# Kernel tuning notes

Measured on AMD Instinct MI355X. Metric: run time of the kernel, lower is better.

The kernel has to match this reference:

```python
import jax, jax.numpy as jnp
import numpy as np

VOCABSIZE = 100000
EMBEDSIZE = 128
BATCH = 262144


def setup_inputs() -> dict:
    key = jax.random.key(0)
    k1, k2, k3, k4, k5 = jax.random.split(key, 5)
    xs = jax.random.randint(k1, (BATCH,), 0, VOCABSIZE, dtype=jnp.int64 if jax.config.jax_enable_x64 else jnp.int32)
    ys = jax.random.randint(k2, (BATCH,), 0, VOCABSIZE, dtype=jnp.int64 if jax.config.jax_enable_x64 else jnp.int32)
    metric = jax.random.normal(k3, (EMBEDSIZE, EMBEDSIZE), dtype=jnp.float32)
    EMBEDM = jax.random.normal(k4, (VOCABSIZE, EMBEDSIZE), dtype=jnp.float32)
    # Original inits NEGEMBEDM to zeros; we use small random values so the
    # output / gradients are non-degenerate for kernel correctness testing.
    NEGEMBEDM = jax.random.normal(k5, (VOCABSIZE, EMBEDSIZE), dtype=jnp.float32) * 0.1
    return {"xs": xs, "ys": ys, "metric": metric, "EMBEDM": EMBEDM, "NEGEMBEDM": NEGEMBEDM}


def reference(xs, ys, metric, EMBEDM, NEGEMBEDM):
    # Faithful math: diag((E[xs] @ metric) @ N[ys].T) == sum((E[xs] @ metric) * N[ys], -1).
    # We compute the batched bilinear form directly, avoiding the O(B^2*D)
    # full matmul + diag extraction of the original.
    xsembeds = EMBEDM[xs]          # [B, D]
    ysembeds = NEGEMBEDM[ys]       # [B, D]
    d = jnp.einsum('bd,de,be->b', xsembeds, metric, ysembeds)  # [B]
    return jax.nn.sigmoid(2.0 * d - 1.0)
```

## Files before the change

### kernel.cpp

```cpp
#include <hip/hip_runtime.h>
#include <hip/hip_fp16.h>

#define D       128
#define NROWS   100000
#define NTILES  (NROWS / 16)
#define NBE     391
#define NBN     (NROWS / 16)
#define NPREP   (NBE + NBN)

typedef __attribute__((ext_vector_type(8))) _Float16 f16x8;
typedef __attribute__((ext_vector_type(4))) float    f32x4;

union F16x8U { _Float16 h[8]; f16x8 v; };
union F32x4U { float f[4]; f32x4 v; };

typedef __attribute__((address_space(1))) const void gvoid;
typedef __attribute__((address_space(3))) void       lvoid;

__global__ __launch_bounds__(256) void convert_M16(
    const float* __restrict__ M, _Float16* __restrict__ mh)
{
    const int q    = blockIdx.x * 256 + threadIdx.x;
    const int kk   = q >> 9;
    const int cf   = (q >> 6) & 7;
    const int lane = q & 63;
    const int col  = cf * 16 + (lane & 15);
    const int k0   = kk * 32 + (lane >> 4) * 8;

    F16x8U h;
    #pragma unroll
    for (int j = 0; j < 8; ++j) h.h[j] = (_Float16)M[(k0 + j) * D + col];
    *(f16x8*)(mh + q * 8) = h.v;
}

__global__ __launch_bounds__(256, 5) void prep_fused(
    const float* __restrict__ E, const float* __restrict__ N,
    const _Float16* __restrict__ mh,
    _Float16* __restrict__ Ep, _Float16* __restrict__ Np)
{
    __shared__ _Float16 sm[2048 * 8];

    const int tid = threadIdx.x;
    const int bid = (int)blockIdx.x;

    if (bid % 17 != 0) {
        const int nid = bid - bid / 17 - 1;
        const int l16 = tid & 15;
        const int row = nid * 16 + (tid >> 4);
        const float* src = N + (size_t)row * D + l16;
        F16x8U o;
        #pragma unroll
        for (int k = 0; k < 8; ++k) o.h[k] = (_Float16)src[16 * k];
        *(f16x8*)(Np + (size_t)row * D + l16 * 8) = o.v;
        return;
    }

    const int eid  = bid / 17;
    const int lane = tid & 63;
    const int w    = tid >> 6;
    const int lrow = lane & 15;
    const int lk   = lane >> 4;

    #pragma unroll
    for (int it = 0; it < 8; ++it) {
        const int slot = it * 256 + w * 64 + lane;
        __builtin_amdgcn_global_load_lds(
            (gvoid*)(mh + slot * 8), (lvoid*)(sm + (it * 256 + w * 64) * 8),
            16, 0, 0);
    }
    asm volatile("s_waitcnt vmcnt(0)" ::: "memory");
    __syncthreads();

    const f16x8* Bh = (const f16x8*)sm;

    #pragma unroll 1
    for (int rt = 0; rt < 4; ++rt) {
        const int tb = eid * 16 + rt * 4 + w;
        if (tb >= NTILES) break;
        const int row = tb * 16 + lrow;

        f32x4 ax[4], ay[4];
        #pragma unroll
        for (int kk = 0; kk < 4; ++kk) {
            const float* p = E + (size_t)row * D + kk * 32 + lk * 8;
            ax[kk] = *(const f32x4*)p;
            ay[kk] = *(const f32x4*)(p + 4);
        }

        f32x4 acc[8];
        #pragma unroll
        for (int cf = 0; cf < 8; ++cf) acc[cf] = (f32x4){0.f, 0.f, 0.f, 0.f};

        #pragma unroll
        for (int kk = 0; kk < 4; ++kk) {
            F16x8U a16;
            F32x4U x, y; x.v = ax[kk]; y.v = ay[kk];
            #pragma unroll
            for (int j = 0; j < 4; ++j) {
                a16.h[j]     = (_Float16)x.f[j];
                a16.h[j + 4] = (_Float16)y.f[j];
            }
            #pragma unroll
            for (int cf = 0; cf < 8; ++cf)
                acc[cf] = __builtin_amdgcn_mfma_f32_16x16x32_f16(
                    a16.v, Bh[(kk * 8 + cf) * 64 + lane], acc[cf], 0, 0, 0);
        }

        #pragma unroll
        for (int i = 0; i < 4; ++i) {
            const int ro = tb * 16 + lk * 4 + i;
            F16x8U o;
            #pragma unroll
            for (int cf = 0; cf < 8; ++cf) o.h[cf] = (_Float16)acc[cf][i];
            *(f16x8*)(Ep + (size_t)ro * D + lrow * 8) = o.v;
        }
    }
}

__global__ __launch_bounds__(256) void gather_dot16(
    const int* __restrict__ xs, const int* __restrict__ ys,
    const _Float16* __restrict__ Ep, const _Float16* __restrict__ Np,
    float* __restrict__ out)
{
    const int tid = threadIdx.x;
    const int o0  = blockIdx.x * 32 + (tid >> 4) * 2;
    const int l   = tid & 15;

    const int x0 = xs[o0], x1 = xs[o0 + 1];
    const int y0 = ys[o0], y1 = ys[o0 + 1];

    const f16x8 a0 = *(const f16x8*)(Ep + (size_t)x0 * D + l * 8);
    const f16x8 b0 = *(const f16x8*)(Np + (size_t)y0 * D + l * 8);
    const f16x8 a1 = *(const f16x8*)(Ep + (size_t)x1 * D + l * 8);
    const f16x8 b1 = *(const f16x8*)(Np + (size_t)y1 * D + l * 8);

    float r0 = 0.f, r1 = 0.f;
    #pragma unroll
    for (int j = 0; j < 8; ++j) {
        r0 += (float)a0[j] * (float)b0[j];
        r1 += (float)a1[j] * (float)b1[j];
    }

    r0 += __shfl_xor(r0, 1); r1 += __shfl_xor(r1, 1);
    r0 += __shfl_xor(r0, 2); r1 += __shfl_xor(r1, 2);
    r0 += __shfl_xor(r0, 4); r1 += __shfl_xor(r1, 4);
    r0 += __shfl_xor(r0, 8); r1 += __shfl_xor(r1, 8);

    if (l == 0) {
        float2 v;
        v.x = 1.0f / (1.0f + __expf(1.0f - 2.0f * r0));
        v.y = 1.0f / (1.0f + __expf(1.0f - 2.0f * r1));
        *(float2*)(out + o0) = v;
    }
}

extern "C" void kernel_launch(void* const* d_in, const int* in_sizes, int n_in,
                              void* d_out, int out_size, void* d_ws, size_t ws_size,
                              hipStream_t stream) {
    const int*   xs     = (const int*)d_in[0];
    const int*   ys     = (const int*)d_in[1];
    const float* metric = (const float*)d_in[2];
    const float* EMBEDM = (const float*)d_in[3];
    const float* NEGEM  = (const float*)d_in[4];
    float*       out    = (float*)d_out;

    const int B = in_sizes[0];

    char* ws = (char*)d_ws;
    _Float16* Np = (_Float16*)ws;
    _Float16* Ep = (_Float16*)(ws + (32u << 20));
    _Float16* mh = (_Float16*)(ws + (64u << 20));

    convert_M16<<<8, 256, 0, stream>>>(metric, mh);

    prep_fused<<<NPREP, 256, 0, stream>>>(EMBEDM, NEGEM, mh, Ep, Np);

    gather_dot16<<<B / 32, 256, 0, stream>>>(xs, ys, Ep, Np, out);
}
```

Measured before the change: 56.27 us.

## Use persistent grid-stride waves for fused E-projection and N-conversion prep

Replaces the one-block-per-work-item prep launch with a fixed 1280-block persistent grid. Each wave strides over a unified list of work units: E tiles that need the MFMA projection, then N row-quads that only need fp16 conversion. The goal is to cut block launch overhead and spread the heavier MFMA tiles across all waves. In exchange, every block now loads the 32KB metric into LDS even if it mostly does N conversion, and the E tiles all come first in the list, which may unbalance work or hurt overlap.

```diff
diff --git a/kernel.cpp b/kernel.cpp
--- a/kernel.cpp
+++ b/kernel.cpp
@@ -1,12 +1,13 @@
 #include <hip/hip_runtime.h>
 #include <hip/hip_fp16.h>
 
-#define D       128
-#define NROWS   100000
-#define NTILES  (NROWS / 16)
-#define NBE     391
-#define NBN     (NROWS / 16)
-#define NPREP   (NBE + NBN)
+#define D        128
+#define NROWS    100000
+#define NET      (NROWS / 16)
+#define NNT      (NROWS / 4)
+#define NUNITS   (NET + NNT)
+#define GRID_P   1280
+#define NWAVES   (GRID_P * 4)
 
 typedef __attribute__((ext_vector_type(8))) _Float16 f16x8;
 typedef __attribute__((ext_vector_type(4))) float    f32x4;
@@ -33,29 +34,14 @@
     *(f16x8*)(mh + q * 8) = h.v;
 }
 
-__global__ __launch_bounds__(256, 5) void prep_fused(
+__global__ __launch_bounds__(256, 5) void prep_all(
     const float* __restrict__ E, const float* __restrict__ N,
     const _Float16* __restrict__ mh,
     _Float16* __restrict__ Ep, _Float16* __restrict__ Np)
 {
     __shared__ _Float16 sm[2048 * 8];
 
-    const int tid = threadIdx.x;
-    const int bid = (int)blockIdx.x;
-
-    if (bid % 17 != 0) {
-        const int nid = bid - bid / 17 - 1;
-        const int l16 = tid & 15;
-        const int row = nid * 16 + (tid >> 4);
-        const float* src = N + (size_t)row * D + l16;
-        F16x8U o;
-        #pragma unroll
-        for (int k = 0; k < 8; ++k) o.h[k] = (_Float16)src[16 * k];
-        *(f16x8*)(Np + (size_t)row * D + l16 * 8) = o.v;
-        return;
-    }
-
-    const int eid  = bid / 17;
+    const int tid  = threadIdx.x;
     const int lane = tid & 63;
     const int w    = tid >> 6;
     const int lrow = lane & 15;
@@ -73,46 +59,55 @@
 
     const f16x8* Bh = (const f16x8*)sm;
 
+    const int gwave = (int)blockIdx.x * 4 + w;
+
     #pragma unroll 1
-    for (int rt = 0; rt < 4; ++rt) {
-        const int tb = eid * 16 + rt * 4 + w;
-        if (tb >= NTILES) break;
-        const int row = tb * 16 + lrow;
+    for (int u = gwave; u < NUNITS; u += NWAVES) {
+        if (u < NET) {
+            const int row = u * 16 + lrow;
 
-        f32x4 ax[4], ay[4];
-        #pragma unroll
-        for (int kk = 0; kk < 4; ++kk) {
-            const float* p = E + (size_t)row * D + kk * 32 + lk * 8;
-            ax[kk] = *(const f32x4*)p;
-            ay[kk] = *(const f32x4*)(p + 4);
-        }
+            f32x4 ax[4], ay[4];
+            #pragma unroll
+            for (int kk = 0; kk < 4; ++kk) {
+                const float* p = E + (size_t)row * D + kk * 32 + lk * 8;
+                ax[kk] = *(const f32x4*)p;
+                ay[kk] = *(const f32x4*)(p + 4);
+            }
 
-        f32x4 acc[8];
-        #pragma unroll
-        for (int cf = 0; cf < 8; ++cf) acc[cf] = (f32x4){0.f, 0.f, 0.f, 0.f};
+            f32x4 acc[8];
+            #pragma unroll
+            for (int cf = 0; cf < 8; ++cf) acc[cf] = (f32x4){0.f, 0.f, 0.f, 0.f};
 
-        #pragma unroll
-        for (int kk = 0; kk < 4; ++kk) {
-            F16x8U a16;
-            F32x4U x, y; x.v = ax[kk]; y.v = ay[kk];
             #pragma unroll
-            for (int j = 0; j < 4; ++j) {
-                a16.h[j]     = (_Float16)x.f[j];
-                a16.h[j + 4] = (_Float16)y.f[j];
+            for (int kk = 0; kk < 4; ++kk) {
+                F16x8U a16;
+                F32x4U x, y; x.v = ax[kk]; y.v = ay[kk];
+                #pragma unroll
+                for (int j = 0; j < 4; ++j) {
+                    a16.h[j]     = (_Float16)x.f[j];
+                    a16.h[j + 4] = (_Float16)y.f[j];
+                }
+                #pragma unroll
+                for (int cf = 0; cf < 8; ++cf)
+                    acc[cf] = __builtin_amdgcn_mfma_f32_16x16x32_f16(
+                        a16.v, Bh[(kk * 8 + cf) * 64 + lane], acc[cf], 0, 0, 0);
             }
+
             #pragma unroll
-            for (int cf = 0; cf < 8; ++cf)
-                acc[cf] = __builtin_amdgcn_mfma_f32_16x16x32_f16(
-                    a16.v, Bh[(kk * 8 + cf) * 64 + lane], acc[cf], 0, 0, 0);
-        }
-
-        #pragma unroll
-        for (int i = 0; i < 4; ++i) {
-            const int ro = tb * 16 + lk * 4 + i;
+            for (int i = 0; i < 4; ++i) {
+                const int ro = u * 16 + lk * 4 + i;
+                F16x8U o;
+                #pragma unroll
+                for (int cf = 0; cf < 8; ++cf) o.h[cf] = (_Float16)acc[cf][i];
+                *(f16x8*)(Ep + (size_t)ro * D + lrow * 8) = o.v;
+            }
+        } else {
+            const int row = (u - NET) * 4 + lk;
+            const float* src = N + (size_t)row * D + lrow;
             F16x8U o;
             #pragma unroll
-            for (int cf = 0; cf < 8; ++cf) o.h[cf] = (_Float16)acc[cf][i];
-            *(f16x8*)(Ep + (size_t)ro * D + lrow * 8) = o.v;
+            for (int k = 0; k < 8; ++k) o.h[k] = (_Float16)src[16 * k];
+            *(f16x8*)(Np + (size_t)row * D + lrow * 8) = o.v;
         }
     }
 }
@@ -173,7 +168,7 @@
 
     convert_M16<<<8, 256, 0, stream>>>(metric, mh);
 
-    prep_fused<<<NPREP, 256, 0, stream>>>(EMBEDM, NEGEM, mh, Ep, Np);
+    prep_all<<<GRID_P, 256, 0, stream>>>(EMBEDM, NEGEM, mh, Ep, Np);
 
     gather_dot16<<<B / 32, 256, 0, stream>>>(xs, ys, Ep, Np, out);
 }
```

New measurement: 53.07 us. 1.06x faster.

## Split fused prep into separate E-GEMM and N-convert kernels with finer GEMM work split

Applied to the files above, without the earlier changes.

Replaces the interleaved fused prep kernel with two launches: a GEMM kernel for E·M using 512-thread blocks where each tile's 8 output column fragments are split across two waves, and a standalone fp16 conversion kernel for N. Each E block now handles 4 tiles in a single pass instead of looping over 16 tiles, so there are more blocks and more waves and less serial work per block. The cost is an extra kernel launch, and the metric matrix is now loaded into LDS by more blocks in total.

```diff
diff --git a/kernel.cpp b/kernel.cpp
--- a/kernel.cpp
+++ b/kernel.cpp
@@ -3,15 +3,16 @@
 
 #define D       128
 #define NROWS   100000
-#define NTILES  (NROWS / 16)
-#define NBE     391
+#define NET     (NROWS / 16)
+#define NBE     ((NET + 3) / 4)
 #define NBN     (NROWS / 16)
-#define NPREP   (NBE + NBN)
 
 typedef __attribute__((ext_vector_type(8))) _Float16 f16x8;
+typedef __attribute__((ext_vector_type(4))) _Float16 f16x4;
 typedef __attribute__((ext_vector_type(4))) float    f32x4;
 
 union F16x8U { _Float16 h[8]; f16x8 v; };
+union F16x4U { _Float16 h[4]; f16x4 v; };
 union F32x4U { float f[4]; f32x4 v; };
 
 typedef __attribute__((address_space(1))) const void gvoid;
@@ -33,88 +34,79 @@
     *(f16x8*)(mh + q * 8) = h.v;
 }
 
-__global__ __launch_bounds__(256, 5) void prep_fused(
-    const float* __restrict__ E, const float* __restrict__ N,
-    const _Float16* __restrict__ mh,
-    _Float16* __restrict__ Ep, _Float16* __restrict__ Np)
+__global__ __launch_bounds__(512, 8) void gemm_E_hi(
+    const float* __restrict__ E, const _Float16* __restrict__ mh,
+    _Float16* __restrict__ Ep)
 {
-    __shared__ _Float16 sm[2048 * 8];
+    __shared__ _Float16 smM[2048 * 8];
 
-    const int tid = threadIdx.x;
-    const int bid = (int)blockIdx.x;
-
-    if (bid % 17 != 0) {
-        const int nid = bid - bid / 17 - 1;
-        const int l16 = tid & 15;
-        const int row = nid * 16 + (tid >> 4);
-        const float* src = N + (size_t)row * D + l16;
-        F16x8U o;
-        #pragma unroll
-        for (int k = 0; k < 8; ++k) o.h[k] = (_Float16)src[16 * k];
-        *(f16x8*)(Np + (size_t)row * D + l16 * 8) = o.v;
-        return;
-    }
-
-    const int eid  = bid / 17;
+    const int tid  = threadIdx.x;
     const int lane = tid & 63;
     const int w    = tid >> 6;
     const int lrow = lane & 15;
     const int lk   = lane >> 4;
 
     #pragma unroll
-    for (int it = 0; it < 8; ++it) {
-        const int slot = it * 256 + w * 64 + lane;
+    for (int it = 0; it < 4; ++it) {
+        const int slot = it * 512 + w * 64 + lane;
         __builtin_amdgcn_global_load_lds(
-            (gvoid*)(mh + slot * 8), (lvoid*)(sm + (it * 256 + w * 64) * 8),
+            (gvoid*)(mh + slot * 8), (lvoid*)(smM + (it * 512 + w * 64) * 8),
             16, 0, 0);
     }
     asm volatile("s_waitcnt vmcnt(0)" ::: "memory");
     __syncthreads();
 
-    const f16x8* Bh = (const f16x8*)sm;
+    const f16x8* Bh = (const f16x8*)smM;
 
-    #pragma unroll 1
-    for (int rt = 0; rt < 4; ++rt) {
-        const int tb = eid * 16 + rt * 4 + w;
-        if (tb >= NTILES) break;
-        const int row = tb * 16 + lrow;
+    const int tile = (int)blockIdx.x * 4 + (w >> 1);
+    if (tile >= NET) return;
+    const int h   = w & 1;
+    const int row = tile * 16 + lrow;
 
-        f32x4 ax[4], ay[4];
+    f32x4 acc[4];
+    #pragma unroll
+    for (int c = 0; c < 4; ++c) acc[c] = (f32x4){0.f, 0.f, 0.f, 0.f};
+
+    #pragma unroll
+    for (int kk = 0; kk < 4; ++kk) {
+        const float* p = E + (size_t)row * D + kk * 32 + lk * 8;
+        F32x4U x, y;
+        x.v = *(const f32x4*)p;
+        y.v = *(const f32x4*)(p + 4);
+        F16x8U a16;
         #pragma unroll
-        for (int kk = 0; kk < 4; ++kk) {
-            const float* p = E + (size_t)row * D + kk * 32 + lk * 8;
-            ax[kk] = *(const f32x4*)p;
-            ay[kk] = *(const f32x4*)(p + 4);
+        for (int j = 0; j < 4; ++j) {
+            a16.h[j]     = (_Float16)x.f[j];
+            a16.h[j + 4] = (_Float16)y.f[j];
         }
-
-        f32x4 acc[8];
         #pragma unroll
-        for (int cf = 0; cf < 8; ++cf) acc[cf] = (f32x4){0.f, 0.f, 0.f, 0.f};
-
-        #pragma unroll
-        for (int kk = 0; kk < 4; ++kk) {
-            F16x8U a16;
-            F32x4U x, y; x.v = ax[kk]; y.v = ay[kk];
-            #pragma unroll
-            for (int j = 0; j < 4; ++j) {
-                a16.h[j]     = (_Float16)x.f[j];
-                a16.h[j + 4] = (_Float16)y.f[j];
-            }
-            #pragma unroll
-            for (int cf = 0; cf < 8; ++cf)
-                acc[cf] = __builtin_amdgcn_mfma_f32_16x16x32_f16(
-                    a16.v, Bh[(kk * 8 + cf) * 64 + lane], acc[cf], 0, 0, 0);
-        }
-
-        #pragma unroll
-        for (int i = 0; i < 4; ++i) {
-            const int ro = tb * 16 + lk * 4 + i;
-            F16x8U o;
-            #pragma unroll
-            for (int cf = 0; cf < 8; ++cf) o.h[cf] = (_Float16)acc[cf][i];
-            *(f16x8*)(Ep + (size_t)ro * D + lrow * 8) = o.v;
+        for (int c = 0; c < 4; ++c) {
+            const int cf = h * 4 + c;
+            acc[c] = __builtin_amdgcn_mfma_f32_16x16x32_f16(
+                a16.v, Bh[(kk * 8 + cf) * 64 + lane], acc[c], 0, 0, 0);
         }
     }
+
+    #pragma unroll
+    for (int i = 0; i < 4; ++i) {
+        const int ro = tile * 16 + lk * 4 + i;
+        F16x4U o;
+        #pragma unroll
+        for (int c = 0; c < 4; ++c) o.h[c] = (_Float16)acc[c][i];
+        *(f16x4*)(Ep + (size_t)ro * D + lrow * 8 + h * 4) = o.v;
+    }
+}
+
+__global__ __launch_bounds__(256, 8) void conv_N(
+    const float* __restrict__ N, _Float16* __restrict__ Np)
+{
+    const int l16 = threadIdx.x & 15;
+    const int row = blockIdx.x * 16 + (threadIdx.x >> 4);
+    const float* src = N + (size_t)row * D + l16;
+    F16x8U o;
+    #pragma unroll
+    for (int k = 0; k < 8; ++k) o.h[k] = (_Float16)src[16 * k];
+    *(f16x8*)(Np + (size_t)row * D + l16 * 8) = o.v;
 }
 
 __global__ __launch_bounds__(256) void gather_dot16(
@@ -173,7 +165,9 @@
 
     convert_M16<<<8, 256, 0, stream>>>(metric, mh);
 
-    prep_fused<<<NPREP, 256, 0, stream>>>(EMBEDM, NEGEM, mh, Ep, Np);
+    gemm_E_hi<<<NBE, 512, 0, stream>>>(EMBEDM, mh, Ep);
+
+    conv_N<<<NBN, 256, 0, stream>>>(NEGEM, Np);
 
     gather_dot16<<<B / 32, 256, 0, stream>>>(xs, ys, Ep, Np, out);
 }
```

After: 60.04 us. 1.07x slower.
